# Optimization experiments

Measured on AMD Instinct MI355X. Metric: run time of the kernel, lower is better.

## Reference

```python
import jax, jax.numpy as jnp
import numpy as np

B, N, E = 8, 20000, 320000
IN_F, EMBED, HIDDEN = 3, 64, 128


def setup_inputs() -> dict:
    key = jax.random.key(0)
    ks = jax.random.split(key, 16)
    w = lambda k, shape: (jax.random.normal(k, shape, jnp.float32) * 0.05)
    return {
        "actions": jax.random.normal(ks[0], (B, N, 2), jnp.float32),
        "node_features": jax.random.normal(ks[1], (B, 1, N), jnp.float32),
        "edge_index": jax.random.randint(ks[2], (B, 2, E), 0, N, dtype=jnp.int64),
        # GINConv 1 MLP: Linear(3, hidden) -> ReLU -> Linear(hidden, embed)
        "c1_w1": w(ks[3], (IN_F, HIDDEN)), "c1_b1": jnp.zeros((HIDDEN,), jnp.float32),
        "c1_w2": w(ks[4], (HIDDEN, EMBED)), "c1_b2": jnp.zeros((EMBED,), jnp.float32),
        # GINConv 2 MLP: Linear(embed, hidden) -> ReLU -> Linear(hidden, embed)
        "c2_w1": w(ks[5], (EMBED, HIDDEN)), "c2_b1": jnp.zeros((HIDDEN,), jnp.float32),
        "c2_w2": w(ks[6], (HIDDEN, EMBED)), "c2_b2": jnp.zeros((EMBED,), jnp.float32),
        # post-pool MLP (num_mlp_layers=1): Linear(embed, hidden)
        "mlp_w": w(ks[7], (EMBED, HIDDEN)), "mlp_b": jnp.zeros((HIDDEN,), jnp.float32),
        # output layer: Linear(hidden, num_nodes)
        "out_w": w(ks[8], (HIDDEN, N)), "out_b": jnp.zeros((N,), jnp.float32),
    }


def _gin_conv(x, src, dst, w1, b1, w2, b2):
    # message = x[src]; aggregate = scatter-sum into dst; eps=0 -> x + agg; then MLP
    num_nodes = x.shape[0]
    agg = jnp.zeros((num_nodes, x.shape[1]), x.dtype).at[dst].add(x[src])
    h = x + agg
    return jax.nn.relu(h @ w1 + b1) @ w2 + b2


def reference(actions, node_features, edge_index,
              c1_w1, c1_b1, c1_w2, c1_b2,
              c2_w1, c2_b1, c2_w2, c2_b2,
              mlp_w, mlp_b, out_w, out_b):
    nf = jnp.squeeze(node_features)                      # [B, N]
    x = jnp.stack((actions[:, :, 0], actions[:, :, 1], nf), axis=2)  # [B, N, 3]
    x = x.reshape(B * N, IN_F)
    # per-batch node-index offsets, then the original's row-major reshape to (2, B*E)
    offs = (jnp.arange(B, dtype=edge_index.dtype) * N)[:, None, None]
    ei = (edge_index + offs).reshape(2, B * E)
    src, dst = ei[0], ei[1]
    # conv layers (eval mode: dropout is identity), outer ReLU after each conv
    x = jax.nn.relu(_gin_conv(x, src, dst, c1_w1, c1_b1, c1_w2, c1_b2))
    x = jax.nn.relu(_gin_conv(x, src, dst, c2_w1, c2_b1, c2_w2, c2_b2))
    # global sum pool: batch ids are contiguous blocks of N nodes
    x = x.reshape(B, N, EMBED).sum(axis=1)               # [B, embed]
    x = jax.nn.relu(x @ mlp_w + mlp_b)                   # [B, hidden]
    return jax.nn.sigmoid(x @ out_w + out_b)             # [B, num_nodes]
```

## Files before the change

### kernel.cpp

```cpp
#include <hip/hip_runtime.h>
#include <cstdint>
#include <cstddef>

#define NBATCH 8
#define NNODE  20000
#define TWO_E  640000
#define NEDGE  2560000
#define BN     160000
#define HN     80000
#define HID    128
#define EMB    64

#define SB     5000
#define SBB    1250
#define NWG    320
#define CHUNK  8000
#define DCAP   80

#define OFF_POOL     0ull
#define ZERO_BYTES   2048ull
#define OFF_CNT      2048ull
#define OFF_TOTAL    6402048ull
#define OFF_BSTART   6422048ull
#define OFF_BINS     6442080ull
#define OFF_AGG1F    16682080ull
#define OFF_AGG2     17642080ull
#define OFF_X1       27882080ull
#define OFF_W1T1     48362080ull
#define OFF_W1HI     48363616ull
#define OFF_W2HI     48380000ull
#define OFF_W1LO     48396384ull
#define OFF_W2LO     48412768ull
#define OFF_Q        48429152ull

using bf16x8 = __attribute__((ext_vector_type(8))) short;
using f32x4  = __attribute__((ext_vector_type(4))) float;

__device__ __forceinline__ float bf2f(unsigned short u) {
    union { unsigned int i; float f; } v; v.i = ((unsigned int)u) << 16; return v.f;
}
__device__ __forceinline__ unsigned short f2bf(float x) {
    union { float f; unsigned int i; } v; v.f = x;
    unsigned int r = v.i + 0x7FFF + ((v.i >> 16) & 1);
    return (unsigned short)(r >> 16);
}
__device__ __forceinline__ unsigned int addbf2(unsigned int a, unsigned int b) {
    float lo = bf2f((unsigned short)(a & 0xFFFF)) + bf2f((unsigned short)(b & 0xFFFF));
    float hi = bf2f((unsigned short)(a >> 16))    + bf2f((unsigned short)(b >> 16));
    return (unsigned int)f2bf(lo) | ((unsigned int)f2bf(hi) << 16);
}
__device__ __forceinline__ int chunk_of(int b) { return (b & 7) * 40 + (b >> 3); }

__global__ void k_transpose(const float* __restrict__ w1, const float* __restrict__ w2,
                            const float* __restrict__ w2b,
                            float* __restrict__ w1t,
                            unsigned short* __restrict__ w1hi, unsigned short* __restrict__ w2hi,
                            unsigned short* __restrict__ w1lo, unsigned short* __restrict__ w2lo) {
    int t = blockIdx.x * blockDim.x + threadIdx.x;
    int stride = gridDim.x * blockDim.x;
    for (int i = t; i < 3 * 128; i += stride) {
        int k = i / 128, j = i % 128;
        w1t[j * 3 + k] = w1[i];
    }
    for (int i = t; i < 8192; i += stride) {
        int j = i & 7, l = (i >> 3) & 63, fid = i >> 9;
        int n16 = fid >> 1, ks = fid & 1;
        int n = n16 * 16 + (l & 15), k = ks * 32 + (l >> 4) * 8 + j;
        float w = w2[k * 128 + n];
        unsigned short hi = f2bf(w);
        w1hi[i] = hi;
        w1lo[i] = f2bf(w - bf2f(hi));
    }
    for (int i = t; i < 8192; i += stride) {
        int j = i & 7, l = (i >> 3) & 63, fid = i >> 9;
        int n16 = fid >> 2, ks = fid & 3;
        int n = n16 * 16 + (l & 15), k = ks * 32 + (l >> 4) * 8 + j;
        float w = w2b[k * 64 + n];
        unsigned short hi = f2bf(w);
        w2hi[i] = hi;
        w2lo[i] = f2bf(w - bf2f(hi));
    }
}

__global__ __launch_bounds__(256) void k_hist(const int* __restrict__ ei,
                                              int* __restrict__ cnt) {
    __shared__ int hist[SB];
    int tid = threadIdx.x, w = chunk_of(blockIdx.x);
    for (int b = tid; b < SB; b += 256) hist[b] = 0;
    __syncthreads();
    for (int i = tid; i < CHUNK; i += 256) {
        int ig = w * CHUNK + i;
        int b = ig / TWO_E;
        int j = ig - b * TWO_E;
        int d4 = b * NNODE + ei[(b + 4) * TWO_E + j];
        atomicAdd(&hist[d4 >> 4], 1);
    }
    __syncthreads();
    for (int b = tid; b < SB; b += 256) cnt[w * SB + b] = hist[b];
}

__global__ __launch_bounds__(256) void k_scanA(int* __restrict__ cnt,
                                               int* __restrict__ total) {
    __shared__ int m[NWG][20];
    int tid = threadIdx.x;
    int b0 = blockIdx.x * 20;
    for (int i = tid; i < NWG * 20; i += 256) {
        int r = i / 20, c = i - r * 20;
        m[r][c] = cnt[r * SB + b0 + c];
    }
    __syncthreads();
    if (tid < 20) {
        int s = 0;
#pragma unroll 8
        for (int r = 0; r < NWG; ++r) { int v = m[r][tid]; m[r][tid] = s; s += v; }
        total[b0 + tid] = s;
    }
    __syncthreads();
    for (int i = tid; i < NWG * 20; i += 256) {
        int r = i / 20, c = i - r * 20;
        cnt[r * SB + b0 + c] = m[r][c];
    }
}

__global__ __launch_bounds__(1024) void k_scanB(const int* __restrict__ total,
                                                int* __restrict__ binStart) {
    __shared__ int tmp[1024];
    int tid = threadIdx.x;
    int v[5], c[5], s = 0;
    if (tid < 1000) {
#pragma unroll
        for (int k = 0; k < 5; ++k) v[k] = total[tid * 5 + k];
#pragma unroll
        for (int k = 0; k < 5; ++k) { c[k] = s; s += v[k]; }
    }
    tmp[tid] = s;
    __syncthreads();
    for (int off = 1; off < 1024; off <<= 1) {
        int t = (tid >= off) ? tmp[tid - off] : 0;
        __syncthreads();
        tmp[tid] += t;
        __syncthreads();
    }
    if (tid < 1000) {
        int excl = tmp[tid] - s;
#pragma unroll
        for (int k = 0; k < 5; ++k) binStart[tid * 5 + k] = excl + c[k];
    }
    if (tid == 0) binStart[SB] = NEDGE;
}

__global__ __launch_bounds__(256) void k_place(const int* __restrict__ ei,
                                               const int* __restrict__ cnt,
                                               const int* __restrict__ binStart,
                                               unsigned int* __restrict__ bins) {
    __shared__ int cur[SB];
    int tid = threadIdx.x, w = chunk_of(blockIdx.x);
    for (int b = tid; b < SB; b += 256) cur[b] = binStart[b] + cnt[w * SB + b];
    __syncthreads();
    for (int i = tid; i < CHUNK; i += 256) {
        int ig = w * CHUNK + i;
        int b = ig / TWO_E;
        int j = ig - b * TWO_E;
        int sn = ei[b * TWO_E + j];
        int d4 = b * NNODE + ei[(b + 4) * TWO_E + j];
        unsigned int e = ((unsigned int)d4 << 15) | (unsigned int)sn;
        int pos = atomicAdd(&cur[d4 >> 4], 1);
        bins[pos] = e;
    }
}

__global__ __launch_bounds__(256) void k_agg1(const unsigned int* __restrict__ bins,
                                              const int* __restrict__ binStart,
                                              const float* __restrict__ actions,
                                              const float* __restrict__ nf,
                                              float* __restrict__ agg1f) {
    int tid = threadIdx.x, lane = tid & 63, wv = tid >> 6;
    int sub = blockIdx.x * 4 + wv;
    int dstBase = sub * 16;
    int batchBase = (dstBase / NNODE) * NNODE;
    int start = binStart[sub];
    int cnt = binStart[sub + 1] - start;
    const float2* act2 = reinterpret_cast<const float2*>(actions);

    float acc[48];
#pragma unroll
    for (int k = 0; k < 48; ++k) acc[k] = 0.0f;

    for (int base = 0; base < cnt; base += 64) {
        int i = base + lane;
        float v0 = 0.f, v1 = 0.f, v2 = 0.f;
        int slot = 16;
        if (i < cnt) {
            unsigned int e = bins[start + i];
            slot = (int)((e >> 15) & 15);
            int s = batchBase + (int)(e & 0x7FFF);
            float2 a = act2[s];
            v0 = a.x; v1 = a.y; v2 = nf[s];
        }
#pragma unroll
        for (int t = 0; t < 16; ++t) {
            bool m = (slot == t);
            acc[t * 3 + 0] += m ? v0 : 0.0f;
            acc[t * 3 + 1] += m ? v1 : 0.0f;
            acc[t * 3 + 2] += m ? v2 : 0.0f;
        }
    }

#pragma unroll
    for (int k = 0; k < 48; ++k) {
        float v = acc[k];
        v += __shfl_xor(v, 1, 64);
        v += __shfl_xor(v, 2, 64);
        v += __shfl_xor(v, 4, 64);
        v += __shfl_xor(v, 8, 64);
        v += __shfl_xor(v, 16, 64);
        v += __shfl_xor(v, 32, 64);
        acc[k] = v;
    }
    float outv = 0.0f;
#pragma unroll
    for (int k = 0; k < 48; ++k) outv = (lane == k) ? acc[k] : outv;
    if (lane < 48) agg1f[dstBase * 3 + lane] = outv;
}

__global__ __launch_bounds__(256) void k_conv1(const float* __restrict__ actions,
                                               const float* __restrict__ nf,
                                               const float* __restrict__ agg1f,
                                               const float* __restrict__ w1t,
                                               const float* __restrict__ b1,
                                               const float* __restrict__ w2,
                                               const float* __restrict__ b2,
                                               unsigned short* __restrict__ x1) {
    int t = blockIdx.x * blockDim.x + threadIdx.x;
    if (t >= BN) return;
    const float2* act2 = reinterpret_cast<const float2*>(actions);
    float2 a = act2[t];
    float h0 = a.x, h1 = a.y, h2 = nf[t];
    if (t >= HN) {
        int d4 = t - HN;
        h0 += agg1f[d4 * 3 + 0];
        h1 += agg1f[d4 * 3 + 1];
        h2 += agg1f[d4 * 3 + 2];
    }

    float acc[64];
#pragma unroll
    for (int o = 0; o < 64; ++o) acc[o] = b2[o];

#pragma unroll 2
    for (int j = 0; j < HID; ++j) {
        float hj = fmaf(h0, w1t[3 * j + 0],
                   fmaf(h1, w1t[3 * j + 1],
                   fmaf(h2, w1t[3 * j + 2], b1[j])));
        hj = fmaxf(hj, 0.0f);
        const float* w2r = w2 + j * 64;
#pragma unroll
        for (int o = 0; o < 64; ++o) acc[o] = fmaf(hj, w2r[o], acc[o]);
    }
    uint4* xo = reinterpret_cast<uint4*>(x1 + (size_t)t * 64);
#pragma unroll
    for (int g = 0; g < 8; ++g) {
        uint4 v;
        v.x = f2bf(fmaxf(acc[8 * g + 0], 0.f)) | ((unsigned int)f2bf(fmaxf(acc[8 * g + 1], 0.f)) << 16);
        v.y = f2bf(fmaxf(acc[8 * g + 2], 0.f)) | ((unsigned int)f2bf(fmaxf(acc[8 * g + 3], 0.f)) << 16);
        v.z = f2bf(fmaxf(acc[8 * g + 4], 0.f)) | ((unsigned int)f2bf(fmaxf(acc[8 * g + 5], 0.f)) << 16);
        v.w = f2bf(fmaxf(acc[8 * g + 6], 0.f)) | ((unsigned int)f2bf(fmaxf(acc[8 * g + 7], 0.f)) << 16);
        xo[g] = v;
    }
}

__global__ __launch_bounds__(256) void k_agg2(const unsigned int* __restrict__ bins,
                                              const int* __restrict__ binStart,
                                              const unsigned short* __restrict__ x1,
                                              unsigned short* __restrict__ agg2) {
    __shared__ unsigned int seg[4][16 * DCAP];
    int tid = threadIdx.x, lane = tid & 63, wv = tid >> 6;
    int xcd = blockIdx.x & 7, jj = blockIdx.x >> 3;
    int batch = xcd >> 1, half = xcd & 1;
    int localSub = (half * 160 + jj) * 4 + wv;
    if (localSub >= SBB) return;
    int sub = batch * SBB + localSub;
    int dstBase = sub * 16;
    int batchBase = batch * NNODE;
    unsigned int* myseg = seg[wv];

    int start = binStart[sub];
    int cnt = binStart[sub + 1] - start;

    int cur[16];
#pragma unroll
    for (int t = 0; t < 16; ++t) cur[t] = 0;
    for (int base = 0; base < cnt; base += 64) {
        int i = base + lane;
        int slot = 16;
        unsigned int e = 0;
        if (i < cnt) { e = bins[start + i]; slot = (int)((e >> 15) & 15); }
        int pos = DCAP;
#pragma unroll
        for (int t = 0; t < 16; ++t) {
            unsigned long long mask = __ballot(slot == t);
            int rank = (int)__popcll(mask & ((1ull << lane) - 1ull));
            pos = (slot == t) ? (cur[t] + rank) : pos;
            cur[t] += (int)__popcll(mask);
        }
        if (i < cnt && pos < DCAP) myseg[slot * DCAP + pos] = e;
    }

#pragma unroll 1
    for (int t = 0; t < 16; ++t) {
        int n = cur[t]; if (n > DCAP) n = DCAP;
        int base = t * DCAP;
        float a0 = 0.f, a1 = 0.f, a2 = 0.f, a3 = 0.f;
        int p = 0;
        for (; p + 4 <= n; p += 4) {
            unsigned int e0 = myseg[base + p],     e1 = myseg[base + p + 1];
            unsigned int e2 = myseg[base + p + 2], e3 = myseg[base + p + 3];
            int s0 = batchBase + (int)(e0 & 0x7FFF);
            int s1 = batchBase + (int)(e1 & 0x7FFF);
            int s2 = batchBase + (int)(e2 & 0x7FFF);
            int s3 = batchBase + (int)(e3 & 0x7FFF);
            a0 += bf2f(x1[(size_t)s0 * 64 + lane]);
            a1 += bf2f(x1[(size_t)s1 * 64 + lane]);
            a2 += bf2f(x1[(size_t)s2 * 64 + lane]);
            a3 += bf2f(x1[(size_t)s3 * 64 + lane]);
        }
        for (; p < n; ++p) {
            unsigned int e0 = myseg[base + p];
            int s0 = batchBase + (int)(e0 & 0x7FFF);
            a0 += bf2f(x1[(size_t)s0 * 64 + lane]);
        }
        agg2[(size_t)(dstBase + t) * 64 + lane] = f2bf((a0 + a1) + (a2 + a3));
    }
}

__global__ __launch_bounds__(256) void k_conv2pool(const unsigned short* __restrict__ x1,
                                                   const unsigned short* __restrict__ agg2,
                                                   const unsigned short* __restrict__ w1hi,
                                                   const unsigned short* __restrict__ w1lo,
                                                   const unsigned short* __restrict__ w2hi,
                                                   const unsigned short* __restrict__ w2lo,
                                                   const float* __restrict__ b1,
                                                   const float* __restrict__ b2,
                                                   float* __restrict__ pool) {
    __shared__ __align__(16) unsigned short Hs[32][72];
    __shared__ __align__(16) unsigned short Hid[32][136];
    __shared__ float poolLDS[64];

    const int tid  = threadIdx.x;
    const int lane = tid & 63;
    const int wv   = tid >> 6;
    const int quad = lane >> 4;
    const int l16  = lane & 15;

    const int m0 = blockIdx.x * 32;
    const int b  = m0 / NNODE;
    const int mt = wv & 1;

    if (tid < 64) poolLDS[tid] = 0.0f;

    {
        int row = tid >> 3, g = tid & 7;
        const uint4* xr = reinterpret_cast<const uint4*>(x1 + (size_t)(m0 + row) * 64 + g * 8);
        uint4 v = *xr;
        if (m0 >= HN) {
            const uint4* ar = reinterpret_cast<const uint4*>(agg2 + (size_t)(m0 - HN + row) * 64 + g * 8);
            uint4 a = *ar;
            v.x = addbf2(v.x, a.x); v.y = addbf2(v.y, a.y);
            v.z = addbf2(v.z, a.z); v.w = addbf2(v.w, a.w);
        }
        *reinterpret_cast<uint4*>(&Hs[row][g * 8]) = v;
    }
    __syncthreads();

    {
        const int nb = (wv >> 1) * 64;
        f32x4 acc[4];
#pragma unroll
        for (int nt = 0; nt < 4; ++nt) acc[nt] = {0.f, 0.f, 0.f, 0.f};
#pragma unroll
        for (int ks = 0; ks < 2; ++ks) {
            bf16x8 h = *reinterpret_cast<const bf16x8*>(&Hs[mt * 16 + l16][ks * 32 + quad * 8]);
#pragma unroll
            for (int nt = 0; nt < 4; ++nt) {
                int fid = ((nb >> 4) + nt) * 2 + ks;
                bf16x8 whi = *reinterpret_cast<const bf16x8*>(&w1hi[(size_t)(fid * 64 + lane) * 8]);
                bf16x8 wlo = *reinterpret_cast<const bf16x8*>(&w1lo[(size_t)(fid * 64 + lane) * 8]);
                acc[nt] = __builtin_amdgcn_mfma_f32_16x16x32_bf16(whi, h, acc[nt], 0, 0, 0);
                acc[nt] = __builtin_amdgcn_mfma_f32_16x16x32_bf16(wlo, h, acc[nt], 0, 0, 0);
            }
        }
#pragma unroll
        for (int nt = 0; nt < 4; ++nt) {
            int hbase = nb + nt * 16 + quad * 4;
            float4 bias = *reinterpret_cast<const float4*>(&b1[hbase]);
            unsigned int p0 = (unsigned int)f2bf(fmaxf(acc[nt][0] + bias.x, 0.0f))
                            | ((unsigned int)f2bf(fmaxf(acc[nt][1] + bias.y, 0.0f)) << 16);
            unsigned int p1 = (unsigned int)f2bf(fmaxf(acc[nt][2] + bias.z, 0.0f))
                            | ((unsigned int)f2bf(fmaxf(acc[nt][3] + bias.w, 0.0f)) << 16);
            uint2 pk; pk.x = p0; pk.y = p1;
            *reinterpret_cast<uint2*>(&Hid[mt * 16 + l16][hbase]) = pk;
        }
    }
    __syncthreads();

    {
        const int nb = (wv >> 1) * 32;
        f32x4 acc[2];
#pragma unroll
        for (int nt = 0; nt < 2; ++nt) acc[nt] = {0.f, 0.f, 0.f, 0.f};
#pragma unroll
        for (int ks = 0; ks < 4; ++ks) {
            bf16x8 a = *reinterpret_cast<const bf16x8*>(&Hid[mt * 16 + l16][ks * 32 + quad * 8]);
#pragma unroll
            for (int nt = 0; nt < 2; ++nt) {
                int fid = ((nb >> 4) + nt) * 4 + ks;
                bf16x8 whi = *reinterpret_cast<const bf16x8*>(&w2hi[(size_t)(fid * 64 + lane) * 8]);
                bf16x8 wlo = *reinterpret_cast<const bf16x8*>(&w2lo[(size_t)(fid * 64 + lane) * 8]);
                acc[nt] = __builtin_amdgcn_mfma_f32_16x16x32_bf16(a, whi, acc[nt], 0, 0, 0);
                acc[nt] = __builtin_amdgcn_mfma_f32_16x16x32_bf16(a, wlo, acc[nt], 0, 0, 0);
            }
        }
#pragma unroll
        for (int nt = 0; nt < 2; ++nt) {
            int n = nb + nt * 16 + l16;
            float bias = b2[n];
            float p = 0.0f;
#pragma unroll
            for (int r = 0; r < 4; ++r) p += fmaxf(acc[nt][r] + bias, 0.0f);
            p += __shfl_xor(p, 16, 64);
            p += __shfl_xor(p, 32, 64);
            if (lane < 16) atomicAdd(&poolLDS[n], p);
        }
    }
    __syncthreads();

    if (tid < 64) atomicAdd(&pool[b * 64 + tid], poolLDS[tid]);
}

__global__ __launch_bounds__(128) void k_q(const float* __restrict__ pool,
                                           const float* __restrict__ mlp_w,
                                           const float* __restrict__ mlp_b,
                                           float* __restrict__ q) {
    int j = threadIdx.x;
    for (int b = 0; b < NBATCH; ++b) {
        float a = mlp_b[j];
#pragma unroll 8
        for (int k = 0; k < 64; ++k) a = fmaf(pool[b * 64 + k], mlp_w[k * 128 + j], a);
        q[b * 128 + j] = fmaxf(a, 0.0f);
    }
}

__global__ __launch_bounds__(256) void k_out(const float* __restrict__ q,
                                             const float* __restrict__ out_w,
                                             const float* __restrict__ out_b,
                                             float* __restrict__ out) {
    __shared__ float qs[NBATCH][128];
    int tid = threadIdx.x;
    for (int i = tid; i < NBATCH * 128; i += 256) qs[i >> 7][i & 127] = q[i];
    __syncthreads();
    int c = tid & 31, b = tid >> 5;
    int n = blockIdx.x * 32 + c;
    const float* qr = qs[b];
    float a = out_b[n];
#pragma unroll 8
    for (int j = 0; j < 128; ++j) a = fmaf(qr[j], out_w[j * NNODE + n], a);
    out[b * NNODE + n] = 1.0f / (1.0f + expf(-a));
}

extern "C" void kernel_launch(void* const* d_in, const int* in_sizes, int n_in,
                              void* d_out, int out_size, void* d_ws, size_t ws_size,
                              hipStream_t stream) {
    const float* actions = (const float*)d_in[0];
    const float* nf      = (const float*)d_in[1];
    const int*   ei      = (const int*)d_in[2];
    const float* c1_w1   = (const float*)d_in[3];
    const float* c1_b1   = (const float*)d_in[4];
    const float* c1_w2   = (const float*)d_in[5];
    const float* c1_b2   = (const float*)d_in[6];
    const float* c2_w1   = (const float*)d_in[7];
    const float* c2_b1   = (const float*)d_in[8];
    const float* c2_w2   = (const float*)d_in[9];
    const float* c2_b2   = (const float*)d_in[10];
    const float* mlp_w   = (const float*)d_in[11];
    const float* mlp_b   = (const float*)d_in[12];
    const float* out_w   = (const float*)d_in[13];
    const float* out_b   = (const float*)d_in[14];
    float* out = (float*)d_out;

    char* ws = (char*)d_ws;
    float*        pool     = (float*)(ws + OFF_POOL);
    int*          cnt      = (int*)(ws + OFF_CNT);
    int*          total    = (int*)(ws + OFF_TOTAL);
    int*          binStart = (int*)(ws + OFF_BSTART);
    unsigned int* bins     = (unsigned int*)(ws + OFF_BINS);
    float*        agg1f    = (float*)(ws + OFF_AGG1F);
    unsigned short* agg2   = (unsigned short*)(ws + OFF_AGG2);
    unsigned short* x1     = (unsigned short*)(ws + OFF_X1);
    float* w1t1 = (float*)(ws + OFF_W1T1);
    unsigned short* w1hi = (unsigned short*)(ws + OFF_W1HI);
    unsigned short* w2hi = (unsigned short*)(ws + OFF_W2HI);
    unsigned short* w1lo = (unsigned short*)(ws + OFF_W1LO);
    unsigned short* w2lo = (unsigned short*)(ws + OFF_W2LO);
    float* q = (float*)(ws + OFF_Q);

    hipMemsetAsync(d_ws, 0, ZERO_BYTES, stream);

    k_transpose<<<32, 256, 0, stream>>>(c1_w1, c2_w1, c2_w2, w1t1, w1hi, w2hi, w1lo, w2lo);

    k_hist <<<NWG, 256, 0, stream>>>(ei, cnt);
    k_scanA<<<SB / 20, 256, 0, stream>>>(cnt, total);
    k_scanB<<<1, 1024, 0, stream>>>(total, binStart);
    k_place<<<NWG, 256, 0, stream>>>(ei, cnt, binStart, bins);

    k_agg1<<<SB / 4, 256, 0, stream>>>(bins, binStart, actions, nf, agg1f);
    k_conv1<<<BN / 256, 256, 0, stream>>>(actions, nf, agg1f, w1t1, c1_b1, c1_w2, c1_b2, x1);
    k_agg2<<<1280, 256, 0, stream>>>(bins, binStart, x1, agg2);

    k_conv2pool<<<BN / 32, 256, 0, stream>>>(x1, agg2, w1hi, w1lo, w2hi, w2lo,
                                             c2_b1, c2_b2, pool);

    k_q<<<1, 128, 0, stream>>>(pool, mlp_w, mlp_b, q);
    k_out<<<NNODE / 32, 256, 0, stream>>>(q, out_w, out_b, out);
}
```

Measured before the change: 383.6 us.

## Use bf16 MFMA with hi/lo split for conv1 MLP; split agg2 destinations across waves

```diff
diff --git a/kernel.cpp b/kernel.cpp
--- a/kernel.cpp
+++ b/kernel.cpp
@@ -31,7 +31,9 @@
 #define OFF_W2HI     48380000ull
 #define OFF_W1LO     48396384ull
 #define OFF_W2LO     48412768ull
-#define OFF_Q        48429152ull
+#define OFF_V2HI     48429152ull
+#define OFF_V2LO     48445536ull
+#define OFF_Q        48461920ull
 
 using bf16x8 = __attribute__((ext_vector_type(8))) short;
 using f32x4  = __attribute__((ext_vector_type(4))) float;
@@ -51,16 +53,26 @@
 }
 __device__ __forceinline__ int chunk_of(int b) { return (b & 7) * 40 + (b >> 3); }
 
-__global__ void k_transpose(const float* __restrict__ w1, const float* __restrict__ w2,
-                            const float* __restrict__ w2b,
+__global__ void k_transpose(const float* __restrict__ w1, const float* __restrict__ v2,
+                            const float* __restrict__ w2, const float* __restrict__ w2b,
                             float* __restrict__ w1t,
-                            unsigned short* __restrict__ w1hi, unsigned short* __restrict__ w2hi,
-                            unsigned short* __restrict__ w1lo, unsigned short* __restrict__ w2lo) {
+                            unsigned short* __restrict__ v2hi, unsigned short* __restrict__ v2lo,
+                            unsigned short* __restrict__ w1hi, unsigned short* __restrict__ w1lo,
+                            unsigned short* __restrict__ w2hi, unsigned short* __restrict__ w2lo) {
     int t = blockIdx.x * blockDim.x + threadIdx.x;
     int stride = gridDim.x * blockDim.x;
     for (int i = t; i < 3 * 128; i += stride) {
         int k = i / 128, j = i % 128;
         w1t[j * 3 + k] = w1[i];
+    }
+    for (int i = t; i < 8192; i += stride) {
+        int j = i & 7, l = (i >> 3) & 63, fid = i >> 9;
+        int n16 = fid >> 2, ks = fid & 3;
+        int n = n16 * 16 + (l & 15), k = ks * 32 + (l >> 4) * 8 + j;
+        float w = v2[k * 64 + n];
+        unsigned short hi = f2bf(w);
+        v2hi[i] = hi;
+        v2lo[i] = f2bf(w - bf2f(hi));
     }
     for (int i = t; i < 8192; i += stride) {
         int j = i & 7, l = (i >> 3) & 63, fid = i >> 9;
@@ -228,44 +240,87 @@
                                                const float* __restrict__ agg1f,
                                                const float* __restrict__ w1t,
                                                const float* __restrict__ b1,
-                                               const float* __restrict__ w2,
+                                               const unsigned short* __restrict__ v2hi,
+                                               const unsigned short* __restrict__ v2lo,
                                                const float* __restrict__ b2,
                                                unsigned short* __restrict__ x1) {
-    int t = blockIdx.x * blockDim.x + threadIdx.x;
-    if (t >= BN) return;
-    const float2* act2 = reinterpret_cast<const float2*>(actions);
-    float2 a = act2[t];
-    float h0 = a.x, h1 = a.y, h2 = nf[t];
-    if (t >= HN) {
-        int d4 = t - HN;
-        h0 += agg1f[d4 * 3 + 0];
-        h1 += agg1f[d4 * 3 + 1];
-        h2 += agg1f[d4 * 3 + 2];
-    }
-
-    float acc[64];
-#pragma unroll
-    for (int o = 0; o < 64; ++o) acc[o] = b2[o];
-
-#pragma unroll 2
-    for (int j = 0; j < HID; ++j) {
-        float hj = fmaf(h0, w1t[3 * j + 0],
-                   fmaf(h1, w1t[3 * j + 1],
-                   fmaf(h2, w1t[3 * j + 2], b1[j])));
-        hj = fmaxf(hj, 0.0f);
-        const float* w2r = w2 + j * 64;
-#pragma unroll
-        for (int o = 0; o < 64; ++o) acc[o] = fmaf(hj, w2r[o], acc[o]);
-    }
-    uint4* xo = reinterpret_cast<uint4*>(x1 + (size_t)t * 64);
-#pragma unroll
-    for (int g = 0; g < 8; ++g) {
-        uint4 v;
-        v.x = f2bf(fmaxf(acc[8 * g + 0], 0.f)) | ((unsigned int)f2bf(fmaxf(acc[8 * g + 1], 0.f)) << 16);
-        v.y = f2bf(fmaxf(acc[8 * g + 2], 0.f)) | ((unsigned int)f2bf(fmaxf(acc[8 * g + 3], 0.f)) << 16);
-        v.z = f2bf(fmaxf(acc[8 * g + 4], 0.f)) | ((unsigned int)f2bf(fmaxf(acc[8 * g + 5], 0.f)) << 16);
-        v.w = f2bf(fmaxf(acc[8 * g + 6], 0.f)) | ((unsigned int)f2bf(fmaxf(acc[8 * g + 7], 0.f)) << 16);
-        xo[g] = v;
+    __shared__ float hL[32][3];
+    __shared__ __align__(16) unsigned short Hid[32][136];
+    const int tid  = threadIdx.x;
+    const int lane = tid & 63;
+    const int wv   = tid >> 6;
+    const int quad = lane >> 4;
+    const int l16  = lane & 15;
+    const int m0   = blockIdx.x * 32;
+
+    if (tid < 32) {
+        int t = m0 + tid;
+        const float2* act2 = reinterpret_cast<const float2*>(actions);
+        float2 a = act2[t];
+        float h0 = a.x, h1 = a.y, h2 = nf[t];
+        if (t >= HN) {
+            int d4 = t - HN;
+            h0 += agg1f[d4 * 3 + 0];
+            h1 += agg1f[d4 * 3 + 1];
+            h2 += agg1f[d4 * 3 + 2];
+        }
+        hL[tid][0] = h0; hL[tid][1] = h1; hL[tid][2] = h2;
+    }
+    __syncthreads();
+
+    {
+        int node = tid >> 3, jg = (tid & 7) * 16;
+        float h0 = hL[node][0], h1 = hL[node][1], h2 = hL[node][2];
+        float vv[16];
+#pragma unroll
+        for (int u = 0; u < 16; ++u) {
+            int j = jg + u;
+            vv[u] = fmaxf(fmaf(h0, w1t[3 * j + 0],
+                          fmaf(h1, w1t[3 * j + 1],
+                          fmaf(h2, w1t[3 * j + 2], b1[j]))), 0.0f);
+        }
+        uint4 A, B;
+        A.x = (unsigned int)f2bf(vv[0])  | ((unsigned int)f2bf(vv[1])  << 16);
+        A.y = (unsigned int)f2bf(vv[2])  | ((unsigned int)f2bf(vv[3])  << 16);
+        A.z = (unsigned int)f2bf(vv[4])  | ((unsigned int)f2bf(vv[5])  << 16);
+        A.w = (unsigned int)f2bf(vv[6])  | ((unsigned int)f2bf(vv[7])  << 16);
+        B.x = (unsigned int)f2bf(vv[8])  | ((unsigned int)f2bf(vv[9])  << 16);
+        B.y = (unsigned int)f2bf(vv[10]) | ((unsigned int)f2bf(vv[11]) << 16);
+        B.z = (unsigned int)f2bf(vv[12]) | ((unsigned int)f2bf(vv[13]) << 16);
+        B.w = (unsigned int)f2bf(vv[14]) | ((unsigned int)f2bf(vv[15]) << 16);
+        *reinterpret_cast<uint4*>(&Hid[node][jg]) = A;
+        *reinterpret_cast<uint4*>(&Hid[node][jg + 8]) = B;
+    }
+    __syncthreads();
+
+    {
+        const int mt = wv & 1;
+        const int nb = (wv >> 1) * 32;
+        f32x4 acc[2];
+#pragma unroll
+        for (int nt = 0; nt < 2; ++nt) acc[nt] = {0.f, 0.f, 0.f, 0.f};
+#pragma unroll
+        for (int ks = 0; ks < 4; ++ks) {
+            bf16x8 a = *reinterpret_cast<const bf16x8*>(&Hid[mt * 16 + l16][ks * 32 + quad * 8]);
+#pragma unroll
+            for (int nt = 0; nt < 2; ++nt) {
+                int fid = ((nb >> 4) + nt) * 4 + ks;
+                bf16x8 whi = *reinterpret_cast<const bf16x8*>(&v2hi[(size_t)(fid * 64 + lane) * 8]);
+                bf16x8 wlo = *reinterpret_cast<const bf16x8*>(&v2lo[(size_t)(fid * 64 + lane) * 8]);
+                acc[nt] = __builtin_amdgcn_mfma_f32_16x16x32_bf16(a, whi, acc[nt], 0, 0, 0);
+                acc[nt] = __builtin_amdgcn_mfma_f32_16x16x32_bf16(a, wlo, acc[nt], 0, 0, 0);
+            }
+        }
+#pragma unroll
+        for (int nt = 0; nt < 2; ++nt) {
+            int n = nb + nt * 16 + l16;
+            float bias = b2[n];
+#pragma unroll
+            for (int r = 0; r < 4; ++r) {
+                int node = mt * 16 + quad * 4 + r;
+                x1[(size_t)(m0 + node) * 64 + n] = f2bf(fmaxf(acc[nt][r] + bias, 0.0f));
+            }
+        }
     }
 }
 
@@ -273,41 +328,49 @@
                                               const int* __restrict__ binStart,
                                               const unsigned short* __restrict__ x1,
                                               unsigned short* __restrict__ agg2) {
-    __shared__ unsigned int seg[4][16 * DCAP];
+    __shared__ unsigned int seg[4][8 * DCAP];
     int tid = threadIdx.x, lane = tid & 63, wv = tid >> 6;
     int xcd = blockIdx.x & 7, jj = blockIdx.x >> 3;
-    int batch = xcd >> 1, half = xcd & 1;
-    int localSub = (half * 160 + jj) * 4 + wv;
-    if (localSub >= SBB) return;
-    int sub = batch * SBB + localSub;
-    int dstBase = sub * 16;
+    int batch = xcd >> 1, halfB = xcd & 1;
+    int local = jj * 2 + (wv >> 1);
+    if (local >= 625) return;
+    int sub = batch * SBB + halfB * 625 + local;
+    int halfD = wv & 1;
+    int dstBase = sub * 16 + halfD * 8;
     int batchBase = batch * NNODE;
     unsigned int* myseg = seg[wv];
 
     int start = binStart[sub];
     int cnt = binStart[sub + 1] - start;
 
-    int cur[16];
-#pragma unroll
-    for (int t = 0; t < 16; ++t) cur[t] = 0;
+    int cur[8];
+#pragma unroll
+    for (int t = 0; t < 8; ++t) cur[t] = 0;
     for (int base = 0; base < cnt; base += 64) {
         int i = base + lane;
-        int slot = 16;
+        int slot = 8;
         unsigned int e = 0;
-        if (i < cnt) { e = bins[start + i]; slot = (int)((e >> 15) & 15); }
+        if (i < cnt) {
+            e = bins[start + i];
+            int s = (int)((e >> 15) & 15) - halfD * 8;
+            slot = ((unsigned)s < 8u) ? s : 8;
+        }
         int pos = DCAP;
-#pragma unroll
-        for (int t = 0; t < 16; ++t) {
+        int st = 8;
+#pragma unroll
+        for (int t = 0; t < 8; ++t) {
             unsigned long long mask = __ballot(slot == t);
             int rank = (int)__popcll(mask & ((1ull << lane) - 1ull));
-            pos = (slot == t) ? (cur[t] + rank) : pos;
+            bool m = (slot == t);
+            pos = m ? (cur[t] + rank) : pos;
+            st  = m ? t : st;
             cur[t] += (int)__popcll(mask);
         }
-        if (i < cnt && pos < DCAP) myseg[slot * DCAP + pos] = e;
+        if (st < 8 && pos < DCAP) myseg[st * DCAP + pos] = e;
     }
 
 #pragma unroll 1
-    for (int t = 0; t < 16; ++t) {
+    for (int t = 0; t < 8; ++t) {
         int n = cur[t]; if (n > DCAP) n = DCAP;
         int base = t * DCAP;
         float a0 = 0.f, a1 = 0.f, a2 = 0.f, a3 = 0.f;
@@ -501,11 +564,14 @@
     unsigned short* w2hi = (unsigned short*)(ws + OFF_W2HI);
     unsigned short* w1lo = (unsigned short*)(ws + OFF_W1LO);
     unsigned short* w2lo = (unsigned short*)(ws + OFF_W2LO);
+    unsigned short* v2hi = (unsigned short*)(ws + OFF_V2HI);
+    unsigned short* v2lo = (unsigned short*)(ws + OFF_V2LO);
     float* q = (float*)(ws + OFF_Q);
 
     hipMemsetAsync(d_ws, 0, ZERO_BYTES, stream);
 
-    k_transpose<<<32, 256, 0, stream>>>(c1_w1, c2_w1, c2_w2, w1t1, w1hi, w2hi, w1lo, w2lo);
+    k_transpose<<<32, 256, 0, stream>>>(c1_w1, c1_w2, c2_w1, c2_w2,
+                                        w1t1, v2hi, v2lo, w1hi, w1lo, w2hi, w2lo);
 
     k_hist <<<NWG, 256, 0, stream>>>(ei, cnt);
     k_scanA<<<SB / 20, 256, 0, stream>>>(cnt, total);
@@ -513,8 +579,9 @@
     k_place<<<NWG, 256, 0, stream>>>(ei, cnt, binStart, bins);
 
     k_agg1<<<SB / 4, 256, 0, stream>>>(bins, binStart, actions, nf, agg1f);
-    k_conv1<<<BN / 256, 256, 0, stream>>>(actions, nf, agg1f, w1t1, c1_b1, c1_w2, c1_b2, x1);
-    k_agg2<<<1280, 256, 0, stream>>>(bins, binStart, x1, agg2);
+    k_conv1<<<BN / 32, 256, 0, stream>>>(actions, nf, agg1f, w1t1, c1_b1,
+                                         v2hi, v2lo, c1_b2, x1);
+    k_agg2<<<2560, 256, 0, stream>>>(bins, binStart, x1, agg2);
 
     k_conv2pool<<<BN / 32, 256, 0, stream>>>(x1, agg2, w1hi, w1lo, w2hi, w2lo,
                                              c2_b1, c2_b2, pool);
```

Result: faster. 359.3 us (-6.3%).
